# Performance work log

Hardware: AMD Instinct MI355X
Metric: run time of the kernel (lower is better)

Reference implementation:

```python
import jax, jax.numpy as jnp
import numpy as np

NUM_NODES = 50000
NUM_EDGES = 800000
IN_CH = 128
OUT_CH = 128


def setup_inputs() -> dict:
    key = jax.random.key(0)
    k1, k2, k3 = jax.random.split(key, 3)
    x = jax.random.normal(k1, (NUM_NODES, IN_CH), dtype=jnp.float32)
    # xavier_uniform-like init for weight
    limit = float(np.sqrt(6.0 / (IN_CH + OUT_CH)))
    weight = jax.random.uniform(k2, (IN_CH, OUT_CH), dtype=jnp.float32, minval=-limit, maxval=limit)
    edge_index = jax.random.randint(k3, (2, NUM_EDGES), 0, NUM_NODES, dtype=jnp.int64)
    return {"x": x, "weight": weight, "edge_index": edge_index}


def reference(x, weight, edge_index):
    # GCN-style layer: out = D^{-1/2} A D^{-1/2} x W, with A built from COO edges
    # (duplicate edges sum, matching torch sparse_coo_tensor coalescing).
    num_nodes = x.shape[0]
    row, col = edge_index[0], edge_index[1]
    ones = jnp.ones(edge_index.shape[1], dtype=x.dtype)
    deg = jax.ops.segment_sum(ones, row, num_segments=num_nodes)  # row-sum of A
    deg = jnp.where(deg == 0, jnp.asarray(1.0, x.dtype), deg)
    dinv = deg ** -0.5  # [N]
    coef = dinv[row] * dinv[col]  # per-edge normalized value [E]
    msgs = x[col] * coef[:, None]  # gather + scale, [E, C_in]
    agg = jax.ops.segment_sum(msgs, row, num_segments=num_nodes)  # scatter-add, [N, C_in]
    return agg @ weight  # [N, C_out]
```

## Files before the change

### kernel.cpp

```cpp
#include <hip/hip_runtime.h>

#define N_NODES 50000
#define N_EDGES 800000
#define CH 128
#define SLOT 64
#define LDP 136
#define GEMM_B ((N_NODES + 63) / 64)
#define DINV_B ((N_NODES + 255) / 256)

typedef __attribute__((ext_vector_type(8))) short bf16x8;
typedef __attribute__((ext_vector_type(4))) float f32x4;

static __device__ inline unsigned f2bf(float f) {
    union { float f; unsigned u; } v; v.f = f;
    unsigned r = v.u + 0x7fff + ((v.u >> 16) & 1);
    return r >> 16;
}
static __device__ inline float bflo(unsigned v) { union { unsigned u; float f; } c; c.u = v << 16; return c.f; }
static __device__ inline float bfhi(unsigned v) { union { unsigned u; float f; } c; c.u = v & 0xffff0000u; return c.f; }

__global__ __launch_bounds__(256) void k_fillP(const int* __restrict__ rowv,
                                               const int* __restrict__ colv,
                                               const float* __restrict__ W,
                                               int* __restrict__ cursor,
                                               unsigned short* __restrict__ csrP,
                                               unsigned short* __restrict__ wht) {
    int tid = blockIdx.x * 256 + threadIdx.x;
    if (tid < N_EDGES) {
        int r = rowv[tid], c = colv[tid];
        int pos = atomicAdd(&cursor[r], 1);
        if (pos < SLOT) csrP[r * SLOT + pos] = (unsigned short)c;
    } else if (tid - N_EDGES < CH * CH) {
        int i = tid - N_EDGES;
        int k = i >> 7, n = i & 127;
        wht[n * CH + k] = (unsigned short)f2bf(W[i]);
    }
}

__global__ __launch_bounds__(256) void k_gemmX(const float* __restrict__ x,
                                               const unsigned short* __restrict__ wht,
                                               const int* __restrict__ cursor,
                                               unsigned short* __restrict__ yh,
                                               float* __restrict__ dinv) {
    if (blockIdx.x >= GEMM_B) {
        int i = (blockIdx.x - GEMM_B) * 256 + threadIdx.x;
        if (i < N_NODES) {
            int d = cursor[i];
            dinv[i] = rsqrtf((float)(d > 0 ? d : 1));
        }
        return;
    }

    __shared__ short sWT[CH * LDP];
    __shared__ short sA[64 * LDP];
    int t = threadIdx.x;
    int row0 = blockIdx.x * 64;

    {
        const uint4* src = (const uint4*)wht;
        for (int i = t; i < CH * CH / 8; i += 256) {
            int r = i >> 4, c = i & 15;
            *(uint4*)&sWT[r * LDP + c * 8] = src[i];
        }
    }
    const float4* A4 = (const float4*)(x + (size_t)row0 * CH);
    for (int i4 = t; i4 < 64 * (CH / 4); i4 += 256) {
        int r = i4 >> 5, c4 = (i4 & 31) * 4;
        float4 v = (row0 + r < N_NODES) ? A4[i4] : make_float4(0.f, 0.f, 0.f, 0.f);
        short* d = &sA[r * LDP + c4];
        d[0] = (short)f2bf(v.x); d[1] = (short)f2bf(v.y);
        d[2] = (short)f2bf(v.z); d[3] = (short)f2bf(v.w);
    }
    __syncthreads();

    int lane = t & 63, w = t >> 6;
    int m = lane & 15, q = lane >> 4;

    bf16x8 afr[4];
    #pragma unroll
    for (int kk = 0; kk < 4; ++kk)
        afr[kk] = *(const bf16x8*)&sA[(16 * w + m) * LDP + kk * 32 + q * 8];

    f32x4 acc[8];
    #pragma unroll
    for (int c = 0; c < 8; ++c) acc[c] = (f32x4){0.f, 0.f, 0.f, 0.f};

    #pragma unroll
    for (int c = 0; c < 8; ++c) {
        #pragma unroll
        for (int kk = 0; kk < 4; ++kk) {
            bf16x8 bfr = *(const bf16x8*)&sWT[(c * 16 + m) * LDP + kk * 32 + q * 8];
            acc[c] = __builtin_amdgcn_mfma_f32_16x16x32_bf16(afr[kk], bfr, acc[c], 0, 0, 0);
        }
    }

    #pragma unroll
    for (int c = 0; c < 8; ++c) {
        #pragma unroll
        for (int r = 0; r < 4; ++r) {
            int orow = row0 + 16 * w + q * 4 + r;
            if (orow < N_NODES)
                yh[(size_t)orow * CH + c * 16 + m] = (unsigned short)f2bf(acc[c][r]);
        }
    }
}

__global__ __launch_bounds__(256) void k_aggP(const int* __restrict__ cursor,
                                              const unsigned short* __restrict__ csrP,
                                              const float* __restrict__ dinv,
                                              const unsigned short* __restrict__ yh,
                                              float* __restrict__ out) {
    int gid = blockIdx.x * 256 + threadIdx.x;
    int n = gid >> 6;
    int lane = threadIdx.x & 63;
    if (n >= N_NODES) return;
    int cnt = cursor[n]; if (cnt > SLOT) cnt = SLOT;
    const unsigned* __restrict__ y2 = (const unsigned*)yh;
    const uint4* __restrict__ crow = (const uint4*)(csrP + (size_t)n * SLOT);
    float ax = 0.f, ay = 0.f;
    int j = 0;
    for (; j + 8 <= cnt; j += 8) {
        uint4 cc = crow[j >> 3];
        int c0 = cc.x & 0xffff, c1 = cc.x >> 16;
        int c2 = cc.y & 0xffff, c3 = cc.y >> 16;
        int c4 = cc.z & 0xffff, c5 = cc.z >> 16;
        int c6 = cc.w & 0xffff, c7 = cc.w >> 16;
        float w0 = dinv[c0], w1 = dinv[c1], w2 = dinv[c2], w3 = dinv[c3];
        float w4 = dinv[c4], w5 = dinv[c5], w6 = dinv[c6], w7 = dinv[c7];
        unsigned v0 = y2[c0 * 64 + lane];
        unsigned v1 = y2[c1 * 64 + lane];
        unsigned v2 = y2[c2 * 64 + lane];
        unsigned v3 = y2[c3 * 64 + lane];
        unsigned v4 = y2[c4 * 64 + lane];
        unsigned v5 = y2[c5 * 64 + lane];
        unsigned v6 = y2[c6 * 64 + lane];
        unsigned v7 = y2[c7 * 64 + lane];
        ax = fmaf(bflo(v0), w0, ax); ay = fmaf(bfhi(v0), w0, ay);
        ax = fmaf(bflo(v1), w1, ax); ay = fmaf(bfhi(v1), w1, ay);
        ax = fmaf(bflo(v2), w2, ax); ay = fmaf(bfhi(v2), w2, ay);
        ax = fmaf(bflo(v3), w3, ax); ay = fmaf(bfhi(v3), w3, ay);
        ax = fmaf(bflo(v4), w4, ax); ay = fmaf(bfhi(v4), w4, ay);
        ax = fmaf(bflo(v5), w5, ax); ay = fmaf(bfhi(v5), w5, ay);
        ax = fmaf(bflo(v6), w6, ax); ay = fmaf(bfhi(v6), w6, ay);
        ax = fmaf(bflo(v7), w7, ax); ay = fmaf(bfhi(v7), w7, ay);
    }
    for (; j < cnt; ++j) {
        int c = csrP[(size_t)n * SLOT + j];
        float w = dinv[c];
        unsigned v = y2[c * 64 + lane];
        ax = fmaf(bflo(v), w, ax); ay = fmaf(bfhi(v), w, ay);
    }
    float dr = dinv[n];
    ((float2*)out)[n * 64 + lane] = make_float2(ax * dr, ay * dr);
}

extern "C" void kernel_launch(void* const* d_in, const int* in_sizes, int n_in,
                              void* d_out, int out_size, void* d_ws, size_t ws_size,
                              hipStream_t stream) {
    const float* x = (const float*)d_in[0];
    const float* W = (const float*)d_in[1];
    const int* edge = (const int*)d_in[2];
    const int* rowv = edge;
    const int* colv = edge + N_EDGES;
    float* out = (float*)d_out;

    char* p = (char*)d_ws;
    int*   cursor = (int*)p;             p += (size_t)N_NODES * 4;
    float* dinv   = (float*)p;           p += (size_t)N_NODES * 4;
    unsigned short* wht  = (unsigned short*)p;     p += (size_t)CH * CH * 2;
    p = (char*)(((uintptr_t)p + 255) & ~(uintptr_t)255);
    unsigned short* csrP = (unsigned short*)p;     p += (size_t)N_NODES * SLOT * 2;
    unsigned short* yh   = (unsigned short*)p;

    hipMemsetAsync(cursor, 0, (size_t)N_NODES * sizeof(int), stream);

    k_fillP<<<(N_EDGES + CH * CH + 255) / 256, 256, 0, stream>>>(rowv, colv, W, cursor, csrP, wht);
    k_gemmX<<<GEMM_B + DINV_B, 256, 0, stream>>>(x, wht, cursor, yh, dinv);
    k_aggP <<<(N_NODES * 64 + 255) / 256, 256, 0, stream>>>(cursor, csrP, dinv, yh, out);
}
```

Measured before the change: 171.6 us.

## Merge CSR fill with GEMM and compute degree normalization inline in aggregation

The edge bucketing and the X·W GEMM now run as independent block ranges of one kernel, dropping a launch and the separate transposed-weight and dinv buffers. The GEMM skips shared memory and loads x rows and W columns straight from global memory, converting them to bf16 in registers. The aggregation recomputes rsqrt of neighbor degrees from cursor rather than reading a precomputed dinv array. The costs are many strided, uncoalesced scalar W loads per MFMA and repeated rsqrt work per edge.

```diff
diff --git a/kernel.cpp b/kernel.cpp
--- a/kernel.cpp
+++ b/kernel.cpp
@@ -4,9 +4,8 @@
 #define N_EDGES 800000
 #define CH 128
 #define SLOT 64
-#define LDP 136
-#define GEMM_B ((N_NODES + 63) / 64)
-#define DINV_B ((N_NODES + 255) / 256)
+#define FB ((N_EDGES + 255) / 256)
+#define GB ((N_NODES + 63) / 64)
 
 typedef __attribute__((ext_vector_type(8))) short bf16x8;
 typedef __attribute__((ext_vector_type(4))) float f32x4;
@@ -19,67 +18,43 @@
 static __device__ inline float bflo(unsigned v) { union { unsigned u; float f; } c; c.u = v << 16; return c.f; }
 static __device__ inline float bfhi(unsigned v) { union { unsigned u; float f; } c; c.u = v & 0xffff0000u; return c.f; }
 
-__global__ __launch_bounds__(256) void k_fillP(const int* __restrict__ rowv,
-                                               const int* __restrict__ colv,
-                                               const float* __restrict__ W,
-                                               int* __restrict__ cursor,
-                                               unsigned short* __restrict__ csrP,
-                                               unsigned short* __restrict__ wht) {
-    int tid = blockIdx.x * 256 + threadIdx.x;
-    if (tid < N_EDGES) {
-        int r = rowv[tid], c = colv[tid];
-        int pos = atomicAdd(&cursor[r], 1);
-        if (pos < SLOT) csrP[r * SLOT + pos] = (unsigned short)c;
-    } else if (tid - N_EDGES < CH * CH) {
-        int i = tid - N_EDGES;
-        int k = i >> 7, n = i & 127;
-        wht[n * CH + k] = (unsigned short)f2bf(W[i]);
-    }
-}
-
-__global__ __launch_bounds__(256) void k_gemmX(const float* __restrict__ x,
-                                               const unsigned short* __restrict__ wht,
-                                               const int* __restrict__ cursor,
-                                               unsigned short* __restrict__ yh,
-                                               float* __restrict__ dinv) {
-    if (blockIdx.x >= GEMM_B) {
-        int i = (blockIdx.x - GEMM_B) * 256 + threadIdx.x;
-        if (i < N_NODES) {
-            int d = cursor[i];
-            dinv[i] = rsqrtf((float)(d > 0 ? d : 1));
+__global__ __launch_bounds__(256) void k_fg(const int* __restrict__ rowv,
+                                            const int* __restrict__ colv,
+                                            const float* __restrict__ x,
+                                            const float* __restrict__ W,
+                                            int* __restrict__ cursor,
+                                            unsigned short* __restrict__ csrP,
+                                            unsigned short* __restrict__ yh) {
+    if (blockIdx.x < FB) {
+        int e = blockIdx.x * 256 + threadIdx.x;
+        if (e < N_EDGES) {
+            int r = rowv[e], c = colv[e];
+            int pos = atomicAdd(&cursor[r], 1);
+            if (pos < SLOT) csrP[r * SLOT + pos] = (unsigned short)c;
         }
         return;
     }
 
-    __shared__ short sWT[CH * LDP];
-    __shared__ short sA[64 * LDP];
+    int row0 = (blockIdx.x - FB) * 64;
     int t = threadIdx.x;
-    int row0 = blockIdx.x * 64;
-
-    {
-        const uint4* src = (const uint4*)wht;
-        for (int i = t; i < CH * CH / 8; i += 256) {
-            int r = i >> 4, c = i & 15;
-            *(uint4*)&sWT[r * LDP + c * 8] = src[i];
-        }
-    }
-    const float4* A4 = (const float4*)(x + (size_t)row0 * CH);
-    for (int i4 = t; i4 < 64 * (CH / 4); i4 += 256) {
-        int r = i4 >> 5, c4 = (i4 & 31) * 4;
-        float4 v = (row0 + r < N_NODES) ? A4[i4] : make_float4(0.f, 0.f, 0.f, 0.f);
-        short* d = &sA[r * LDP + c4];
-        d[0] = (short)f2bf(v.x); d[1] = (short)f2bf(v.y);
-        d[2] = (short)f2bf(v.z); d[3] = (short)f2bf(v.w);
-    }
-    __syncthreads();
-
     int lane = t & 63, w = t >> 6;
     int m = lane & 15, q = lane >> 4;
 
+    int row = row0 + 16 * w + m;
+    int rc = row < N_NODES ? row : N_NODES - 1;
+    const float4* xr = (const float4*)(x + (size_t)rc * CH);
     bf16x8 afr[4];
     #pragma unroll
-    for (int kk = 0; kk < 4; ++kk)
-        afr[kk] = *(const bf16x8*)&sA[(16 * w + m) * LDP + kk * 32 + q * 8];
+    for (int kk = 0; kk < 4; ++kk) {
+        float4 a0 = xr[kk * 8 + q * 2];
+        float4 a1 = xr[kk * 8 + q * 2 + 1];
+        bf16x8 a;
+        a[0] = (short)f2bf(a0.x); a[1] = (short)f2bf(a0.y);
+        a[2] = (short)f2bf(a0.z); a[3] = (short)f2bf(a0.w);
+        a[4] = (short)f2bf(a1.x); a[5] = (short)f2bf(a1.y);
+        a[6] = (short)f2bf(a1.z); a[7] = (short)f2bf(a1.w);
+        afr[kk] = a;
+    }
 
     f32x4 acc[8];
     #pragma unroll
@@ -87,10 +62,15 @@
 
     #pragma unroll
     for (int c = 0; c < 8; ++c) {
+        int n = c * 16 + m;
         #pragma unroll
         for (int kk = 0; kk < 4; ++kk) {
-            bf16x8 bfr = *(const bf16x8*)&sWT[(c * 16 + m) * LDP + kk * 32 + q * 8];
-            acc[c] = __builtin_amdgcn_mfma_f32_16x16x32_bf16(afr[kk], bfr, acc[c], 0, 0, 0);
+            int k0 = kk * 32 + q * 8;
+            bf16x8 b;
+            #pragma unroll
+            for (int j = 0; j < 8; ++j)
+                b[j] = (short)f2bf(W[(size_t)(k0 + j) * CH + n]);
+            acc[c] = __builtin_amdgcn_mfma_f32_16x16x32_bf16(afr[kk], b, acc[c], 0, 0, 0);
         }
     }
 
@@ -105,16 +85,17 @@
     }
 }
 
-__global__ __launch_bounds__(256) void k_aggP(const int* __restrict__ cursor,
-                                              const unsigned short* __restrict__ csrP,
-                                              const float* __restrict__ dinv,
-                                              const unsigned short* __restrict__ yh,
-                                              float* __restrict__ out) {
+__global__ __launch_bounds__(256) void k_agg(const int* __restrict__ cursor,
+                                             const unsigned short* __restrict__ csrP,
+                                             const unsigned short* __restrict__ yh,
+                                             float* __restrict__ out) {
     int gid = blockIdx.x * 256 + threadIdx.x;
     int n = gid >> 6;
     int lane = threadIdx.x & 63;
     if (n >= N_NODES) return;
-    int cnt = cursor[n]; if (cnt > SLOT) cnt = SLOT;
+    int deg = cursor[n];
+    int cnt = deg < SLOT ? deg : SLOT;
+    float dr = rsqrtf((float)(deg > 0 ? deg : 1));
     const unsigned* __restrict__ y2 = (const unsigned*)yh;
     const uint4* __restrict__ crow = (const uint4*)(csrP + (size_t)n * SLOT);
     float ax = 0.f, ay = 0.f;
@@ -125,8 +106,16 @@
         int c2 = cc.y & 0xffff, c3 = cc.y >> 16;
         int c4 = cc.z & 0xffff, c5 = cc.z >> 16;
         int c6 = cc.w & 0xffff, c7 = cc.w >> 16;
-        float w0 = dinv[c0], w1 = dinv[c1], w2 = dinv[c2], w3 = dinv[c3];
-        float w4 = dinv[c4], w5 = dinv[c5], w6 = dinv[c6], w7 = dinv[c7];
+        int d0 = cursor[c0], d1 = cursor[c1], d2 = cursor[c2], d3 = cursor[c3];
+        int d4 = cursor[c4], d5 = cursor[c5], d6 = cursor[c6], d7 = cursor[c7];
+        float w0 = rsqrtf((float)(d0 > 0 ? d0 : 1));
+        float w1 = rsqrtf((float)(d1 > 0 ? d1 : 1));
+        float w2 = rsqrtf((float)(d2 > 0 ? d2 : 1));
+        float w3 = rsqrtf((float)(d3 > 0 ? d3 : 1));
+        float w4 = rsqrtf((float)(d4 > 0 ? d4 : 1));
+        float w5 = rsqrtf((float)(d5 > 0 ? d5 : 1));
+        float w6 = rsqrtf((float)(d6 > 0 ? d6 : 1));
+        float w7 = rsqrtf((float)(d7 > 0 ? d7 : 1));
         unsigned v0 = y2[c0 * 64 + lane];
         unsigned v1 = y2[c1 * 64 + lane];
         unsigned v2 = y2[c2 * 64 + lane];
@@ -146,11 +135,11 @@
     }
     for (; j < cnt; ++j) {
         int c = csrP[(size_t)n * SLOT + j];
-        float w = dinv[c];
+        int d = cursor[c];
+        float wc = rsqrtf((float)(d > 0 ? d : 1));
         unsigned v = y2[c * 64 + lane];
-        ax = fmaf(bflo(v), w, ax); ay = fmaf(bfhi(v), w, ay);
+        ax = fmaf(bflo(v), wc, ax); ay = fmaf(bfhi(v), wc, ay);
     }
-    float dr = dinv[n];
     ((float2*)out)[n * 64 + lane] = make_float2(ax * dr, ay * dr);
 }
 
@@ -165,16 +154,13 @@
     float* out = (float*)d_out;
 
     char* p = (char*)d_ws;
-    int*   cursor = (int*)p;             p += (size_t)N_NODES * 4;
-    float* dinv   = (float*)p;           p += (size_t)N_NODES * 4;
-    unsigned short* wht  = (unsigned short*)p;     p += (size_t)CH * CH * 2;
+    int* cursor = (int*)p;                         p += (size_t)N_NODES * 4;
     p = (char*)(((uintptr_t)p + 255) & ~(uintptr_t)255);
     unsigned short* csrP = (unsigned short*)p;     p += (size_t)N_NODES * SLOT * 2;
     unsigned short* yh   = (unsigned short*)p;
 
     hipMemsetAsync(cursor, 0, (size_t)N_NODES * sizeof(int), stream);
 
-    k_fillP<<<(N_EDGES + CH * CH + 255) / 256, 256, 0, stream>>>(rowv, colv, W, cursor, csrP, wht);
-    k_gemmX<<<GEMM_B + DINV_B, 256, 0, stream>>>(x, wht, cursor, yh, dinv);
-    k_aggP <<<(N_NODES * 64 + 255) / 256, 256, 0, stream>>>(cursor, csrP, dinv, yh, out);
+    k_fg <<<FB + GB, 256, 0, stream>>>(rowv, colv, x, W, cursor, csrP, yh);
+    k_agg<<<(N_NODES * 64 + 255) / 256, 256, 0, stream>>>(cursor, csrP, yh, out);
 }
```

After: 182.6 us. 6.4% more time.
